# Kernel tuning notes

Measured on AMD Instinct MI355X. Metric: run time of the kernel, lower is better.

The kernel has to match this reference:

```python
import jax, jax.numpy as jnp
import numpy as np
from jax.scipy.special import logsumexp

# Complete binary tree, heap indexing: node i has children 2i+1, 2i+2.
# Edge for child c (c >= 1) is edge_pot[c-1], shape [C, C]:
#   rows = parent state, cols = child state (matches torch code's
#   logsumexp(edge + msg, dim=1) upward and edge.T downward).
DEPTH = 18
C = 16
N = 2 ** (DEPTH + 1) - 1  # 524287 nodes, N-1 edges


def setup_inputs() -> dict:
    key = jax.random.key(0)
    k1, k2 = jax.random.split(key)
    unary = jax.random.normal(k1, (N, C), dtype=jnp.float32)
    edge_pot = jax.random.normal(k2, (N - 1, C, C), dtype=jnp.float32)
    return {"unary": unary, "edge_pot": edge_pot, "depth": DEPTH}


def reference(unary, edge_pot, depth):
    """Sum-product belief propagation on a complete binary tree.

    Returns beliefs [N, C]: for each node v,
      belief[v] = unary[v] + sum(up messages from children) + down message from parent,
    identical to the per-message torch BFS loop, but processed level-parallel.
    """
    c = unary.shape[1]
    # ---------- upward pass (leaves -> root) ----------
    # subtotal[v] = unary[v] + sum of up-messages from v's children (V2F to parent factor)
    subtotal = unary
    m_up = jnp.zeros_like(unary)  # m_up[ch] = F2V message from edge (parent, ch) to parent
    for d in range(depth, 0, -1):
        lo, hi = 2 ** d - 1, 2 ** (d + 1) - 1          # children level, size 2^d
        ep = edge_pot[lo - 1:hi - 1]                    # [2^d, C, C]
        # logsumexp over child state (axis 2): torch's logsumexp(edge + msg, dim=1)
        msg = logsumexp(ep + subtotal[lo:hi][:, None, :], axis=2)  # [2^d, C]
        m_up = m_up.at[lo:hi].set(msg)
        plo, phi = 2 ** (d - 1) - 1, 2 ** d - 1
        # children of consecutive parents are consecutive pairs (2p+1, 2p+2)
        subtotal = subtotal.at[plo:phi].add(msg.reshape(-1, 2, c).sum(axis=1))
    # ---------- downward pass (root -> leaves) ----------
    m_down = jnp.zeros_like(unary)  # m_down[ch] = F2V message from edge (parent, ch) to ch
    for d in range(1, depth + 1):
        lo, hi = 2 ** d - 1, 2 ** (d + 1) - 1
        plo, phi = 2 ** (d - 1) - 1, 2 ** d - 1
        # V2F from parent p towards child ch: all incoming F2V at p except m_up[ch]
        par_total = jnp.repeat(subtotal[plo:phi] + m_down[plo:phi], 2, axis=0)  # [2^d, C]
        v2f = par_total - m_up[lo:hi]
        ep_t = jnp.swapaxes(edge_pot[lo - 1:hi - 1], 1, 2)  # edge.T: [2^d, Cchild, Cparent]
        msg = logsumexp(ep_t + v2f[:, None, :], axis=2)     # logsumexp over parent state
        m_down = m_down.at[lo:hi].set(msg)
    return subtotal + m_down  # beliefs [N, C]
```

## Files before the change

kernel.cpp:

```cpp
#include <hip/hip_runtime.h>
#include <stdint.h>


#define EPC 256

__device__ __forceinline__ void ldvec16(const float* p, float* d) {
    const float4* q = (const float4*)p;
    #pragma unroll
    for (int t = 0; t < 4; ++t) {
        float4 a = q[t];
        d[4*t+0] = a.x; d[4*t+1] = a.y; d[4*t+2] = a.z; d[4*t+3] = a.w;
    }
}

__device__ __forceinline__ float lse16_rs(const float* r, const float* s) {
    float v[16];
    float m;
    #pragma unroll
    for (int j = 0; j < 16; ++j) {
        v[j] = r[j] + s[j];
        m = (j == 0) ? v[0] : fmaxf(m, v[j]);
    }
    float acc = 0.f;
    #pragma unroll
    for (int j = 0; j < 16; ++j) acc += __expf(v[j] - m);
    return m + __logf(acc);
}

__device__ __forceinline__ void enc_row(uint8_t* dst, const float* E) {
    int w[4];
    #pragma unroll
    for (int t = 0; t < 4; ++t) {
        int x = __builtin_amdgcn_cvt_pk_fp8_f32(E[4*t+0], E[4*t+1], 0, false);
        x     = __builtin_amdgcn_cvt_pk_fp8_f32(E[4*t+2], E[4*t+3], x, true);
        w[t] = x;
    }
    *(int4*)dst = make_int4(w[0], w[1], w[2], w[3]);
}

__device__ __forceinline__ void dec_row(const uint8_t* src, float* E) {
    uint4 w = *(const uint4*)src;
    uint32_t a;
    a = w.x;
    E[0]  = __builtin_amdgcn_cvt_f32_fp8(a, 0);
    E[1]  = __builtin_amdgcn_cvt_f32_fp8(a, 1);
    E[2]  = __builtin_amdgcn_cvt_f32_fp8(a, 2);
    E[3]  = __builtin_amdgcn_cvt_f32_fp8(a, 3);
    a = w.y;
    E[4]  = __builtin_amdgcn_cvt_f32_fp8(a, 0);
    E[5]  = __builtin_amdgcn_cvt_f32_fp8(a, 1);
    E[6]  = __builtin_amdgcn_cvt_f32_fp8(a, 2);
    E[7]  = __builtin_amdgcn_cvt_f32_fp8(a, 3);
    a = w.z;
    E[8]  = __builtin_amdgcn_cvt_f32_fp8(a, 0);
    E[9]  = __builtin_amdgcn_cvt_f32_fp8(a, 1);
    E[10] = __builtin_amdgcn_cvt_f32_fp8(a, 2);
    E[11] = __builtin_amdgcn_cvt_f32_fp8(a, 3);
    a = w.w;
    E[12] = __builtin_amdgcn_cvt_f32_fp8(a, 0);
    E[13] = __builtin_amdgcn_cvt_f32_fp8(a, 1);
    E[14] = __builtin_amdgcn_cvt_f32_fp8(a, 2);
    E[15] = __builtin_amdgcn_cvt_f32_fp8(a, 3);
}

__device__ __forceinline__ float dec1(uint8_t b) {
    return __builtin_amdgcn_cvt_f32_fp8((uint32_t)b, 0);
}

__device__ __forceinline__ uint16_t f32_to_bf16(float x) {
    uint32_t u = __float_as_uint(x);
    u += 0x7fff + ((u >> 16) & 1);
    return (uint16_t)(u >> 16);
}
__device__ __forceinline__ float bf16_to_f32(uint16_t h) {
    return __uint_as_float((uint32_t)h << 16);
}

template <bool USE8>
__global__ __launch_bounds__(256) void up_flat(
    const float* __restrict__ csrc, const float* __restrict__ unary,
    const float* __restrict__ ep, float* __restrict__ out,
    uint8_t* __restrict__ e8, uint16_t* __restrict__ mup,
    int plo, int pcount) {
    int t = blockIdx.x * 256 + threadIdx.x;
    if (t >= pcount * 16) return;
    int i = t & 15;
    size_t p = (size_t)plo + (t >> 4);
    size_t cl = 2 * p + 1;

    float msg[2];
    #pragma unroll
    for (int ch = 0; ch < 2; ++ch) {
        size_t c = cl + ch;
        float s[16], r[16];
        ldvec16(csrc + c * 16, s);
        ldvec16(ep + (c - 1) * 256 + i * 16, r);
        if (USE8) {
            float E[16];
            #pragma unroll
            for (int j = 0; j < 16; ++j) E[j] = __expf(r[j]);
            enc_row(e8 + (c - 1) * EPC + i * 16, E);
            float m = s[0];
            #pragma unroll
            for (int j = 1; j < 16; ++j) m = fmaxf(m, s[j]);
            float acc = 0.f;
            #pragma unroll
            for (int j = 0; j < 16; ++j) acc += E[j] * __expf(s[j] - m);
            msg[ch] = __logf(acc) + m;
            mup[c * 16 + i] = f32_to_bf16(msg[ch]);
        } else {
            msg[ch] = lse16_rs(r, s);
        }
    }
    out[p * 16 + i] = unary[p * 16 + i] + msg[0] + msg[1];
}

template <bool USE8>
__global__ __launch_bounds__(256) void down_flat(
    const float* __restrict__ ssrc, const float* __restrict__ ep,
    const uint8_t* __restrict__ e8, const uint16_t* __restrict__ mup,
    float* __restrict__ out, int lo, int count) {
    if (!USE8) {
        int t = blockIdx.x * 256 + threadIdx.x;
        if (t >= count * 16) return;
        int i = t & 15;
        size_t v = (size_t)lo + (t >> 4);
        size_t par = (v - 1) >> 1;
        float s[16], r[16];
        ldvec16(ssrc + v * 16, s);
        float sub_i = ssrc[v * 16 + i];
        ldvec16(ep + (v - 1) * 256 + i * 16, r);
        float mu = lse16_rs(r, s);
        float v2f = out[par * 16 + i] - mu;
        const float* nb = ep + (v - 1) * 256 + i;
        float c[16];
        #pragma unroll
        for (int k = 0; k < 16; ++k) c[k] = nb[k * 16];
        float vv[16], m;
        #pragma unroll
        for (int k = 0; k < 16; ++k) {
            float x = c[k] + __shfl(v2f, k, 16);
            vv[k] = x;
            m = (k == 0) ? x : fmaxf(m, x);
        }
        float acc = 0.f;
        #pragma unroll
        for (int k = 0; k < 16; ++k) acc += __expf(vv[k] - m);
        out[v * 16 + i] = sub_i + m + __logf(acc);
        return;
    }
    __shared__ float T[16][16][20];
    int g = threadIdx.x >> 4, i = threadIdx.x & 15;
    size_t v = (size_t)lo + (size_t)(blockIdx.x * 16 + g);
    size_t par = (v - 1) >> 1;

    float sub_i = ssrc[v * 16 + i];
    float pt    = out[par * 16 + i];
    float mu    = bf16_to_f32(mup[v * 16 + i]);
    float v2f   = pt - mu;

    float m = v2f;
    m = fmaxf(m, __shfl_xor(m, 1, 16));
    m = fmaxf(m, __shfl_xor(m, 2, 16));
    m = fmaxf(m, __shfl_xor(m, 4, 16));
    m = fmaxf(m, __shfl_xor(m, 8, 16));
    float u = __expf(v2f - m);

    float E[16];
    dec_row(e8 + (v - 1) * EPC + i * 16, E);
    #pragma unroll
    for (int j = 0; j < 16; ++j) T[g][i][j] = E[j] * u;
    __syncthreads();
    float acc = 0.f;
    #pragma unroll
    for (int k = 0; k < 16; ++k) acc += T[g][k][i];

    out[v * 16 + i] = sub_i + __logf(acc) + m;
}

__global__ __launch_bounds__(1024) void top6(const float* __restrict__ unary,
                                             const float* __restrict__ ep,
                                             float* __restrict__ out) {
    __shared__ uint8_t epl[126 * 256];
    __shared__ float sb[127][16];
    __shared__ float mu[127][16];
    __shared__ float un[63][16];
    int tid = threadIdx.x;

    for (int row = tid; row < 126 * 16; row += 1024) {
        float r[16], E[16];
        ldvec16(ep + (size_t)row * 16, r);
        #pragma unroll
        for (int j = 0; j < 16; ++j) E[j] = __expf(r[j]);
        enc_row(&epl[row * 16], E);
    }
    {
        int g = tid >> 4, i = tid & 15;
        sb[63 + g][i] = out[(size_t)(63 + g) * 16 + i];
    }
    if (tid < 63 * 16) un[tid >> 4][tid & 15] = unary[tid];
    __syncthreads();

    #pragma unroll
    for (int d = 6; d >= 1; --d) {
        int pcount = 1 << (d - 1);
        if (tid < pcount * 16) {
            int pl = tid >> 4, i = tid & 15;
            int p = pcount - 1 + pl;
            float msg[2];
            #pragma unroll
            for (int ch = 0; ch < 2; ++ch) {
                int c = 2 * p + 1 + ch;
                float E[16], s[16];
                dec_row(&epl[(c - 1) * 256 + i * 16], E);
                ldvec16(&sb[c][0], s);
                float m = s[0];
                #pragma unroll
                for (int j = 1; j < 16; ++j) m = fmaxf(m, s[j]);
                float acc = 0.f;
                #pragma unroll
                for (int j = 0; j < 16; ++j) acc += E[j] * __expf(s[j] - m);
                msg[ch] = __logf(acc) + m;
                mu[c][i] = msg[ch];
            }
            sb[p][i] = un[p][i] + msg[0] + msg[1];
        }
        __syncthreads();
    }

    #pragma unroll
    for (int d = 1; d <= 6; ++d) {
        int count = 1 << d;
        if (tid < count * 16) {
            int vl = tid >> 4, i = tid & 15;
            int v = count - 1 + vl;
            int par = (v - 1) >> 1;
            float v2f = sb[par][i] - mu[v][i];
            float m = v2f;
            m = fmaxf(m, __shfl_xor(m, 1, 16));
            m = fmaxf(m, __shfl_xor(m, 2, 16));
            m = fmaxf(m, __shfl_xor(m, 4, 16));
            m = fmaxf(m, __shfl_xor(m, 8, 16));
            float u = __expf(v2f - m);
            const uint8_t* nb = &epl[(v - 1) * 256];
            float acc = 0.f;
            #pragma unroll
            for (int k = 0; k < 16; ++k)
                acc += dec1(nb[k * 16 + i]) * __shfl(u, k, 16);
            float bel = sb[v][i] + __logf(acc) + m;
            sb[v][i] = bel;
        }
        __syncthreads();
    }

    const float* sbf = &sb[0][0];
    for (int t = tid; t < 127 * 16; t += 1024) out[t] = sbf[t];
}

__device__ __forceinline__ void up_body_f32(const float* __restrict__ unary,
                                            const float* __restrict__ ep,
                                            float* out, size_t p, int i) {
    size_t cl = 2 * p + 1, cr = cl + 1;
    float s[16], r[16];
    ldvec16(out + cl * 16, s);
    ldvec16(ep + (cl - 1) * 256 + i * 16, r);
    float msgL = lse16_rs(r, s);
    ldvec16(out + cr * 16, s);
    ldvec16(ep + (cr - 1) * 256 + i * 16, r);
    float msgR = lse16_rs(r, s);
    out[p * 16 + i] = unary[p * 16 + i] + msgL + msgR;
}

__device__ __forceinline__ void down_body_f32(const float* __restrict__ ep,
                                              float* out, size_t v, int i) {
    size_t par = (v - 1) >> 1;
    float s[16], r[16];
    ldvec16(out + v * 16, s);
    float sub_i = out[v * 16 + i];
    ldvec16(ep + (v - 1) * 256 + i * 16, r);
    float mu = lse16_rs(r, s);
    float v2f = out[par * 16 + i] - mu;
    const float* nb = ep + (v - 1) * 256 + i;
    float c[16];
    #pragma unroll
    for (int k = 0; k < 16; ++k) c[k] = nb[k * 16];
    float vv[16], m;
    #pragma unroll
    for (int k = 0; k < 16; ++k) {
        float x = c[k] + __shfl(v2f, k, 16);
        vv[k] = x;
        m = (k == 0) ? x : fmaxf(m, x);
    }
    float acc = 0.f;
    #pragma unroll
    for (int k = 0; k < 16; ++k) acc += __expf(vv[k] - m);
    out[v * 16 + i] = sub_i + m + __logf(acc);
}

__global__ __launch_bounds__(1024) void top_fused(const float* __restrict__ unary,
                                                  const float* __restrict__ ep,
                                                  float* out, int FD) {
    int tid = threadIdx.x;
    for (int d = FD; d >= 1; --d) {
        int pcount = 1 << (d - 1);
        size_t plo = pcount - 1;
        for (int t = tid; t < pcount * 16; t += blockDim.x)
            up_body_f32(unary, ep, out, plo + (t >> 4), t & 15);
        __syncthreads();
    }
    for (int d = 1; d <= FD; ++d) {
        int count = 1 << d;
        size_t lo = count - 1;
        for (int t = tid; t < count * 16; t += blockDim.x)
            down_body_f32(ep, out, lo + (t >> 4), t & 15);
        __syncthreads();
    }
}

extern "C" void kernel_launch(void* const* d_in, const int* in_sizes, int n_in,
                              void* d_out, int out_size, void* d_ws, size_t ws_size,
                              hipStream_t stream) {
    const float* unary = (const float*)d_in[0];
    const float* ep    = (const float*)d_in[1];
    float* out = (float*)d_out;

    int Nn = in_sizes[0] / 16;
    int depth = 0;
    while ((1 << (depth + 1)) < Nn + 1) ++depth;

    uint8_t* e8 = (uint8_t*)d_ws;
    size_t e8_bytes = (size_t)Nn * EPC;
    size_t mup_off = (e8_bytes + 255) & ~(size_t)255;
    uint16_t* mup = (uint16_t*)((uint8_t*)d_ws + mup_off);
    size_t need = mup_off + (size_t)Nn * 16 * 2;
    bool use8 = ws_size >= need;

    if (use8 && depth >= 13) {
        for (int d = depth; d >= 7; --d) {
            int pcount = 1 << (d - 1);
            const float* csrc = (d == depth) ? unary : out;
            up_flat<true><<<pcount * 16 / 256, 256, 0, stream>>>(
                csrc, unary, ep, out, e8, mup, pcount - 1, pcount);
        }
        top6<<<1, 1024, 0, stream>>>(unary, ep, out);
        for (int d = 7; d <= depth; ++d) {
            int count = 1 << d;
            const float* ssrc = (d == depth) ? unary : out;
            down_flat<true><<<count * 16 / 256, 256, 0, stream>>>(
                ssrc, ep, e8, mup, out, count - 1, count);
        }
    } else {
        int FD = (depth >= 2) ? ((depth - 1 < 6) ? depth - 1 : 6) : 0;
        for (int d = depth; d > FD; --d) {
            int pcount = 1 << (d - 1);
            int plo = pcount - 1;
            const float* csrc = (d == depth) ? unary : out;
            dim3 grid((pcount * 16 + 255) / 256);
            up_flat<false><<<grid, 256, 0, stream>>>(
                csrc, unary, ep, out, e8, mup, plo, pcount);
        }
        if (FD > 0)
            top_fused<<<1, 1024, 0, stream>>>(unary, ep, out, FD);
        for (int d = FD + 1; d <= depth; ++d) {
            int count = 1 << d;
            int lo = count - 1;
            const float* ssrc = (d == depth) ? unary : out;
            dim3 grid((count * 16 + 255) / 256);
            down_flat<false><<<grid, 256, 0, stream>>>(
                ssrc, ep, e8, mup, out, lo, count);
        }
    }
}
```

Baseline: 252.8 us.

## Fuse two tree levels per launch in upward and downward passes

```diff
diff --git a/kernel.cpp b/kernel.cpp
--- a/kernel.cpp
+++ b/kernel.cpp
@@ -76,6 +76,126 @@
     return __uint_as_float((uint32_t)h << 16);
 }
 
+__device__ __forceinline__ float up_edge_gsrc(
+    const float* __restrict__ src16, const float* __restrict__ eprow,
+    uint8_t* __restrict__ e8row, uint16_t* __restrict__ mup1) {
+    float s[16], r[16], E[16];
+    ldvec16(src16, s);
+    ldvec16(eprow, r);
+    #pragma unroll
+    for (int j = 0; j < 16; ++j) E[j] = __expf(r[j]);
+    enc_row(e8row, E);
+    float m = s[0];
+    #pragma unroll
+    for (int j = 1; j < 16; ++j) m = fmaxf(m, s[j]);
+    float acc = 0.f;
+    #pragma unroll
+    for (int j = 0; j < 16; ++j) acc += E[j] * __expf(s[j] - m);
+    float msg = __logf(acc) + m;
+    *mup1 = f32_to_bf16(msg);
+    return msg;
+}
+
+__device__ __forceinline__ float down_edge(
+    float* Tg, int i, float sub_i, float pt, uint16_t mu16,
+    const uint8_t* __restrict__ e8node) {
+    float v2f = pt - bf16_to_f32(mu16);
+    float m = v2f;
+    m = fmaxf(m, __shfl_xor(m, 1, 16));
+    m = fmaxf(m, __shfl_xor(m, 2, 16));
+    m = fmaxf(m, __shfl_xor(m, 4, 16));
+    m = fmaxf(m, __shfl_xor(m, 8, 16));
+    float u = __expf(v2f - m);
+    float E[16];
+    dec_row(e8node + i * 16, E);
+    #pragma unroll
+    for (int j = 0; j < 16; ++j) Tg[i * 20 + j] = E[j] * u;
+    float acc = 0.f;
+    #pragma unroll
+    for (int k = 0; k < 16; ++k) acc += Tg[k * 20 + i];
+    return sub_i + __logf(acc) + m;
+}
+
+__global__ __launch_bounds__(256) void up_bi(
+    const float* __restrict__ gcsrc, const float* __restrict__ unary,
+    const float* __restrict__ ep, float* __restrict__ out,
+    uint8_t* __restrict__ e8, uint16_t* __restrict__ mup,
+    int gplo, int gpcount) {
+    __shared__ float ubuf[16][16];
+    int t = blockIdx.x * 256 + threadIdx.x;
+    if (t >= gpcount * 16) return;
+    int i = t & 15;
+    int g = threadIdx.x >> 4;
+    size_t gp = (size_t)gplo + (t >> 4);
+
+    float msgc[2];
+    #pragma unroll
+    for (int ch = 0; ch < 2; ++ch) {
+        size_t c = 2 * gp + 1 + ch;
+        float acc_msg = 0.f;
+        #pragma unroll
+        for (int q = 0; q < 2; ++q) {
+            size_t gc = 2 * c + 1 + q;
+            acc_msg += up_edge_gsrc(gcsrc + gc * 16,
+                                    ep + (gc - 1) * 256 + i * 16,
+                                    e8 + (gc - 1) * EPC + i * 16,
+                                    mup + gc * 16 + i);
+        }
+        float subc = unary[c * 16 + i] + acc_msg;
+        out[c * 16 + i] = subc;
+
+        float m = subc;
+        m = fmaxf(m, __shfl_xor(m, 1, 16));
+        m = fmaxf(m, __shfl_xor(m, 2, 16));
+        m = fmaxf(m, __shfl_xor(m, 4, 16));
+        m = fmaxf(m, __shfl_xor(m, 8, 16));
+        float u = __expf(subc - m);
+        ubuf[g][i] = u;
+        float uv[16];
+        ldvec16(&ubuf[g][0], uv);
+
+        float r[16], E[16];
+        ldvec16(ep + (c - 1) * 256 + i * 16, r);
+        #pragma unroll
+        for (int j = 0; j < 16; ++j) E[j] = __expf(r[j]);
+        enc_row(e8 + (c - 1) * EPC + i * 16, E);
+        float acc = 0.f;
+        #pragma unroll
+        for (int j = 0; j < 16; ++j) acc += E[j] * uv[j];
+        msgc[ch] = __logf(acc) + m;
+        mup[c * 16 + i] = f32_to_bf16(msgc[ch]);
+    }
+    out[gp * 16 + i] = unary[gp * 16 + i] + msgc[0] + msgc[1];
+}
+
+__global__ __launch_bounds__(256) void down_bi(
+    const float* __restrict__ gcsrc, const uint8_t* __restrict__ e8,
+    const uint16_t* __restrict__ mup, float* __restrict__ out,
+    int gplo, int gpcount) {
+    __shared__ float T[16 * 325];
+    int t = blockIdx.x * 256 + threadIdx.x;
+    if (t >= gpcount * 16) return;
+    int i = t & 15;
+    float* Tg = &T[(threadIdx.x >> 4) * 325];
+    size_t gp = (size_t)gplo + (t >> 4);
+
+    float ptgp = out[gp * 16 + i];
+    #pragma unroll
+    for (int ch = 0; ch < 2; ++ch) {
+        size_t c = 2 * gp + 1 + ch;
+        float bel_c = down_edge(Tg, i, out[c * 16 + i], ptgp,
+                                mup[c * 16 + i], e8 + (c - 1) * EPC);
+        out[c * 16 + i] = bel_c;
+        #pragma unroll
+        for (int q = 0; q < 2; ++q) {
+            size_t gc = 2 * c + 1 + q;
+            float bel_gc = down_edge(Tg, i, gcsrc[gc * 16 + i], bel_c,
+                                     mup[gc * 16 + i], e8 + (gc - 1) * EPC);
+            out[gc * 16 + i] = bel_gc;
+        }
+    }
+}
+
 template <bool USE8>
 __global__ __launch_bounds__(256) void up_flat(
     const float* __restrict__ csrc, const float* __restrict__ unary,
@@ -92,23 +212,13 @@
     #pragma unroll
     for (int ch = 0; ch < 2; ++ch) {
         size_t c = cl + ch;
-        float s[16], r[16];
-        ldvec16(csrc + c * 16, s);
-        ldvec16(ep + (c - 1) * 256 + i * 16, r);
         if (USE8) {
-            float E[16];
-            #pragma unroll
-            for (int j = 0; j < 16; ++j) E[j] = __expf(r[j]);
-            enc_row(e8 + (c - 1) * EPC + i * 16, E);
-            float m = s[0];
-            #pragma unroll
-            for (int j = 1; j < 16; ++j) m = fmaxf(m, s[j]);
-            float acc = 0.f;
-            #pragma unroll
-            for (int j = 0; j < 16; ++j) acc += E[j] * __expf(s[j] - m);
-            msg[ch] = __logf(acc) + m;
-            mup[c * 16 + i] = f32_to_bf16(msg[ch]);
+            msg[ch] = up_edge_gsrc(csrc + c * 16, ep + (c - 1) * 256 + i * 16,
+                                   e8 + (c - 1) * EPC + i * 16, mup + c * 16 + i);
         } else {
+            float s[16], r[16];
+            ldvec16(csrc + c * 16, s);
+            ldvec16(ep + (c - 1) * 256 + i * 16, r);
             msg[ch] = lse16_rs(r, s);
         }
     }
@@ -149,33 +259,16 @@
         out[v * 16 + i] = sub_i + m + __logf(acc);
         return;
     }
-    __shared__ float T[16][16][20];
-    int g = threadIdx.x >> 4, i = threadIdx.x & 15;
-    size_t v = (size_t)lo + (size_t)(blockIdx.x * 16 + g);
+    __shared__ float T[16 * 325];
+    int t = blockIdx.x * 256 + threadIdx.x;
+    if (t >= count * 16) return;
+    int i = t & 15;
+    float* Tg = &T[(threadIdx.x >> 4) * 325];
+    size_t v = (size_t)lo + (t >> 4);
     size_t par = (v - 1) >> 1;
-
-    float sub_i = ssrc[v * 16 + i];
-    float pt    = out[par * 16 + i];
-    float mu    = bf16_to_f32(mup[v * 16 + i]);
-    float v2f   = pt - mu;
-
-    float m = v2f;
-    m = fmaxf(m, __shfl_xor(m, 1, 16));
-    m = fmaxf(m, __shfl_xor(m, 2, 16));
-    m = fmaxf(m, __shfl_xor(m, 4, 16));
-    m = fmaxf(m, __shfl_xor(m, 8, 16));
-    float u = __expf(v2f - m);
-
-    float E[16];
-    dec_row(e8 + (v - 1) * EPC + i * 16, E);
-    #pragma unroll
-    for (int j = 0; j < 16; ++j) T[g][i][j] = E[j] * u;
-    __syncthreads();
-    float acc = 0.f;
-    #pragma unroll
-    for (int k = 0; k < 16; ++k) acc += T[g][k][i];
-
-    out[v * 16 + i] = sub_i + __logf(acc) + m;
+    float bel = down_edge(Tg, i, ssrc[v * 16 + i], out[par * 16 + i],
+                          mup[v * 16 + i], e8 + (v - 1) * EPC);
+    out[v * 16 + i] = bel;
 }
 
 __global__ __launch_bounds__(1024) void top6(const float* __restrict__ unary,
@@ -336,18 +429,32 @@
     bool use8 = ws_size >= need;
 
     if (use8 && depth >= 13) {
-        for (int d = depth; d >= 7; --d) {
-            int pcount = 1 << (d - 1);
-            const float* csrc = (d == depth) ? unary : out;
+        int lv = depth;
+        for (; lv >= 8; lv -= 2) {
+            int gp = lv - 2;
+            int gpcount = 1 << gp;
+            const float* gcsrc = (lv == depth) ? unary : out;
+            up_bi<<<gpcount * 16 / 256, 256, 0, stream>>>(
+                gcsrc, unary, ep, out, e8, mup, gpcount - 1, gpcount);
+        }
+        if (lv == 7) {
+            int pcount = 1 << 6;
             up_flat<true><<<pcount * 16 / 256, 256, 0, stream>>>(
-                csrc, unary, ep, out, e8, mup, pcount - 1, pcount);
+                out, unary, ep, out, e8, mup, pcount - 1, pcount);
         }
         top6<<<1, 1024, 0, stream>>>(unary, ep, out);
-        for (int d = 7; d <= depth; ++d) {
-            int count = 1 << d;
-            const float* ssrc = (d == depth) ? unary : out;
+        int gp0 = 6;
+        if (lv == 7) {
+            int count = 1 << 7;
             down_flat<true><<<count * 16 / 256, 256, 0, stream>>>(
-                ssrc, ep, e8, mup, out, count - 1, count);
+                out, ep, e8, mup, out, count - 1, count);
+            gp0 = 7;
+        }
+        for (int gp = gp0; gp + 2 <= depth; gp += 2) {
+            int gpcount = 1 << gp;
+            const float* gcsrc = (gp + 2 == depth) ? unary : out;
+            down_bi<<<gpcount * 16 / 256, 256, 0, stream>>>(
+                gcsrc, e8, mup, out, gpcount - 1, gpcount);
         }
     } else {
         int FD = (depth >= 2) ? ((depth - 1 < 6) ? depth - 1 : 6) : 0;
```

Result: slower. 265.1 us (+4.9%).
